# Performance work log

Hardware: AMD Instinct MI355X
Metric: run time of the kernel (lower is better)

## Reference

```python
import jax, jax.numpy as jnp
import numpy as np

E = 100000   # n_entities
R = 64       # n_relations
I = 256      # in_channels
O = 256      # out_channels
N_EDGES = 1_600_000


def setup_inputs() -> dict:
    key = jax.random.key(0)
    k1, k2, k3, k4 = jax.random.split(key, 4)
    x = jax.random.normal(k1, (E, I), dtype=jnp.float32)
    # cs must be nonzero (it is reciprocated); uniform in [0.5, 1.5)
    cs = jax.random.uniform(k2, (E, R), dtype=jnp.float32) + 0.5
    W = jax.random.normal(k3, (R, I, O), dtype=jnp.float32) * 0.05
    edge_index = jax.random.randint(k4, (2, N_EDGES), 0, E, dtype=jnp.int64)
    return {"x": x, "cs": cs, "W": W, "edge_index": edge_index}


def reference(x, cs, W, edge_index):
    # Faithful to: torch.einsum('er,rio,ej->eo', 1/cs, W, x)
    # i and j are independently contracted indices, so this factorizes:
    # out[e,o] = (sum_j x[e,j]) * sum_r (1/cs[e,r]) * (sum_i W[r,i,o])
    cs_reciprocal = 1.0 / cs                 # (E, R)
    W_sum = jnp.sum(W, axis=1)               # (R, O)
    x_sum = jnp.sum(x, axis=1)               # (E,)
    src = (cs_reciprocal @ W_sum) * x_sum[:, None]  # (E, O)
    return src
```

## Files before the change

### kernel.cpp

```cpp
#include <hip/hip_runtime.h>


constexpr int En = 100000;
constexpr int Rn = 64;
constexpr int In = 256;
constexpr int On = 256;

__global__ void wsum_kernel(const float* __restrict__ W, float* __restrict__ wsum) {
    const int r = blockIdx.x >> 3;
    const int chunk = blockIdx.x & 7;
    const int o = threadIdx.x;
    const float* base = W + ((size_t)r * In + (size_t)chunk * 32) * On + o;
    float s = 0.f;
#pragma unroll
    for (int i = 0; i < 32; ++i) s += base[(size_t)i * On];
    atomicAdd(&wsum[r * On + o], s);
}

__global__ __launch_bounds__(256) void rgcn_main(const float* __restrict__ x,
                                                 const float* __restrict__ cs,
                                                 const float* __restrict__ wsum,
                                                 float* __restrict__ out) {
    __shared__ float ldsW[Rn * On];
    __shared__ float recipT[Rn * 64];

    const int t = threadIdx.x;
    const int R0 = blockIdx.x * 64;

#pragma unroll
    for (int k = 0; k < 16; ++k) {
        const int f = k * 1024 + t * 4;
        *reinterpret_cast<float4*>(&ldsW[f]) =
            *reinterpret_cast<const float4*>(&wsum[f]);
    }

    const int wv = t >> 6;
    const int lane = t & 63;
#pragma unroll
    for (int s = 0; s < 16; ++s) {
        const int lr = s * 4 + wv;
        const int g = R0 + lr;
        float4 v = make_float4(0.f, 0.f, 0.f, 0.f);
        if (g < En)
            v = *reinterpret_cast<const float4*>(&x[(size_t)g * In + lane * 4]);
        float sum = v.x + v.y + v.z + v.w;
#pragma unroll
        for (int off = 32; off; off >>= 1) sum += __shfl_down(sum, off, 64);
        if (lane == 0) recipT[lr] = sum;
    }
    __syncthreads();

    const int q = t >> 4;
    const int m = t & 15;
    float xs[4];
    float4 c4[4];
#pragma unroll
    for (int s = 0; s < 4; ++s) {
        const int row = s * 16 + q;
        const int g = R0 + row;
        xs[s] = (g < En) ? recipT[row] : 0.f;
        c4[s] = make_float4(1.f, 1.f, 1.f, 1.f);
        if (g < En)
            c4[s] = *reinterpret_cast<const float4*>(&cs[(size_t)g * Rn + m * 4]);
    }
    __syncthreads();

#pragma unroll
    for (int s = 0; s < 4; ++s) {
        const int row = s * 16 + q;
        recipT[(4 * m + 0) * 64 + row] = xs[s] / c4[s].x;
        recipT[(4 * m + 1) * 64 + row] = xs[s] / c4[s].y;
        recipT[(4 * m + 2) * 64 + row] = xs[s] / c4[s].z;
        recipT[(4 * m + 3) * 64 + row] = xs[s] / c4[s].w;
    }
    __syncthreads();

    const int trow = t >> 5;
    const int tcol = t & 31;
    float acc[8][8];
#pragma unroll
    for (int j = 0; j < 8; ++j)
#pragma unroll
        for (int k = 0; k < 8; ++k) acc[j][k] = 0.f;

#pragma unroll 4
    for (int r = 0; r < 64; ++r) {
        const float4 a0 = *reinterpret_cast<float4*>(&recipT[r * 64 + trow * 8]);
        const float4 a1 = *reinterpret_cast<float4*>(&recipT[r * 64 + trow * 8 + 4]);
        const float4 b0 = *reinterpret_cast<float4*>(&ldsW[r * 256 + tcol * 4]);
        const float4 b1 = *reinterpret_cast<float4*>(&ldsW[r * 256 + 128 + tcol * 4]);
        const float a[8] = {a0.x, a0.y, a0.z, a0.w, a1.x, a1.y, a1.z, a1.w};
        const float b[8] = {b0.x, b0.y, b0.z, b0.w, b1.x, b1.y, b1.z, b1.w};
#pragma unroll
        for (int j = 0; j < 8; ++j)
#pragma unroll
            for (int k = 0; k < 8; ++k)
                acc[j][k] = fmaf(a[j], b[k], acc[j][k]);
    }

#pragma unroll
    for (int j = 0; j < 8; ++j) {
        const int g = R0 + trow * 8 + j;
        if (g < En) {
            const float4 o0 = make_float4(acc[j][0], acc[j][1], acc[j][2], acc[j][3]);
            const float4 o1 = make_float4(acc[j][4], acc[j][5], acc[j][6], acc[j][7]);
            *reinterpret_cast<float4*>(&out[(size_t)g * On + tcol * 4]) = o0;
            *reinterpret_cast<float4*>(&out[(size_t)g * On + 128 + tcol * 4]) = o1;
        }
    }
}

extern "C" void kernel_launch(void* const* d_in, const int* in_sizes, int n_in,
                              void* d_out, int out_size, void* d_ws, size_t ws_size,
                              hipStream_t stream) {
    const float* x  = (const float*)d_in[0];
    const float* cs = (const float*)d_in[1];
    const float* W  = (const float*)d_in[2];
    float* wsum = (float*)d_ws;
    float* out  = (float*)d_out;

    hipMemsetAsync(wsum, 0, Rn * On * sizeof(float), stream);
    wsum_kernel<<<dim3(Rn * 8), dim3(256), 0, stream>>>(W, wsum);
    const int tiles = (En + 63) / 64;
    rgcn_main<<<dim3(tiles), dim3(256), 0, stream>>>(x, cs, wsum, out);
}
```

Before: 267.7 us.

## Use bf16 MFMA for reciprocal-by-Wsum GEMM and drop atomics in W reduction

```diff
diff --git a/kernel.cpp b/kernel.cpp
--- a/kernel.cpp
+++ b/kernel.cpp
@@ -6,106 +6,156 @@
 constexpr int In = 256;
 constexpr int On = 256;
 
-__global__ void wsum_kernel(const float* __restrict__ W, float* __restrict__ wsum) {
-    const int r = blockIdx.x >> 3;
-    const int chunk = blockIdx.x & 7;
-    const int o = threadIdx.x;
-    const float* base = W + ((size_t)r * In + (size_t)chunk * 32) * On + o;
-    float s = 0.f;
-#pragma unroll
-    for (int i = 0; i < 32; ++i) s += base[(size_t)i * On];
-    atomicAdd(&wsum[r * On + o], s);
+typedef short bf16x8 __attribute__((ext_vector_type(8)));
+typedef float floatx4 __attribute__((ext_vector_type(4)));
+
+static __device__ __forceinline__ short f2bf(float f) {
+    unsigned u = __builtin_bit_cast(unsigned, f);
+    unsigned r = (u + 0x7FFFu + ((u >> 16) & 1u)) >> 16;
+    return (short)r;
 }
 
-__global__ __launch_bounds__(256) void rgcn_main(const float* __restrict__ x,
-                                                 const float* __restrict__ cs,
-                                                 const float* __restrict__ wsum,
-                                                 float* __restrict__ out) {
-    __shared__ float ldsW[Rn * On];
-    __shared__ float recipT[Rn * 64];
+__global__ __launch_bounds__(256) void wsum_partial(const float* __restrict__ W,
+                                                    float* __restrict__ partial) {
+    const int b = blockIdx.x;
+    const int r = b >> 2;
+    const int qc = b & 3;
+    const int o = threadIdx.x;
+    const float* base = W + ((size_t)r * In + (size_t)qc * 64) * On + o;
+    float s0 = 0.f, s1 = 0.f, s2 = 0.f, s3 = 0.f;
+#pragma unroll
+    for (int i = 0; i < 64; i += 4) {
+        s0 += base[(size_t)(i + 0) * On];
+        s1 += base[(size_t)(i + 1) * On];
+        s2 += base[(size_t)(i + 2) * On];
+        s3 += base[(size_t)(i + 3) * On];
+    }
+    partial[b * On + o] = (s0 + s1) + (s2 + s3);
+}
+
+__global__ __launch_bounds__(256) void wsum_combine(const float* __restrict__ partial,
+                                                    short* __restrict__ wsumT) {
+    const int r = blockIdx.x;
+    const int o = threadIdx.x;
+    const float* p = partial + (size_t)r * 4 * On + o;
+    float s = (p[0] + p[On]) + (p[2 * On] + p[3 * On]);
+    wsumT[o * Rn + r] = f2bf(s);
+}
+
+__global__ __launch_bounds__(256) void wsum_direct(const float* __restrict__ W,
+                                                   short* __restrict__ wsumT) {
+    const int r = blockIdx.x;
+    const int o = threadIdx.x;
+    const float* base = W + (size_t)r * In * On + o;
+    float s0 = 0.f, s1 = 0.f, s2 = 0.f, s3 = 0.f;
+#pragma unroll 16
+    for (int i = 0; i < 256; i += 4) {
+        s0 += base[(size_t)(i + 0) * On];
+        s1 += base[(size_t)(i + 1) * On];
+        s2 += base[(size_t)(i + 2) * On];
+        s3 += base[(size_t)(i + 3) * On];
+    }
+    wsumT[o * Rn + r] = f2bf((s0 + s1) + (s2 + s3));
+}
+
+__global__ __launch_bounds__(256, 3) void rgcn_main(const float* __restrict__ x,
+                                                    const float* __restrict__ cs,
+                                                    const short* __restrict__ wsumT,
+                                                    float* __restrict__ out) {
+    __shared__ __align__(16) short BT[On][72];
+    __shared__ __align__(16) short A[64][72];
+    __shared__ float xs[64];
 
     const int t = threadIdx.x;
     const int R0 = blockIdx.x * 64;
 
+    {
+        const floatx4* wq = (const floatx4*)wsumT;
 #pragma unroll
-    for (int k = 0; k < 16; ++k) {
-        const int f = k * 1024 + t * 4;
-        *reinterpret_cast<float4*>(&ldsW[f]) =
-            *reinterpret_cast<const float4*>(&wsum[f]);
+        for (int k = 0; k < 8; ++k) {
+            const int ch = t + 256 * k;
+            const int o = ch >> 3, seg = ch & 7;
+            *(floatx4*)((char*)&BT[o][0] + seg * 16) = wq[ch];
+        }
     }
 
-    const int wv = t >> 6;
-    const int lane = t & 63;
+    {
+        const int m = t >> 2;
+        const int kc = (t & 3) << 4;
+        const int g = R0 + m;
+        float c[16];
 #pragma unroll
-    for (int s = 0; s < 16; ++s) {
-        const int lr = s * 4 + wv;
-        const int g = R0 + lr;
-        float4 v = make_float4(0.f, 0.f, 0.f, 0.f);
-        if (g < En)
-            v = *reinterpret_cast<const float4*>(&x[(size_t)g * In + lane * 4]);
-        float sum = v.x + v.y + v.z + v.w;
+        for (int j = 0; j < 16; ++j) c[j] = 1.f;
+        if (g < En) {
+            const float4* p = (const float4*)&cs[(size_t)g * Rn + kc];
+            float4 c0 = p[0], c1 = p[1], c2 = p[2], c3 = p[3];
+            c[0] = c0.x; c[1] = c0.y; c[2] = c0.z; c[3] = c0.w;
+            c[4] = c1.x; c[5] = c1.y; c[6] = c1.z; c[7] = c1.w;
+            c[8] = c2.x; c[9] = c2.y; c[10] = c2.z; c[11] = c2.w;
+            c[12] = c3.x; c[13] = c3.y; c[14] = c3.z; c[15] = c3.w;
+        }
+        bf16x8 pk0, pk1;
 #pragma unroll
-        for (int off = 32; off; off >>= 1) sum += __shfl_down(sum, off, 64);
-        if (lane == 0) recipT[lr] = sum;
+        for (int j = 0; j < 8; ++j) {
+            pk0[j] = (g < En) ? f2bf(1.f / c[j]) : (short)0;
+            pk1[j] = (g < En) ? f2bf(1.f / c[8 + j]) : (short)0;
+        }
+        *(bf16x8*)&A[m][kc] = pk0;
+        *(bf16x8*)&A[m][kc + 8] = pk1;
     }
+
+    {
+        const int wv = t >> 6;
+        const int lane = t & 63;
+#pragma unroll
+        for (int s = 0; s < 16; ++s) {
+            const int lr = s * 4 + wv;
+            const int g = R0 + lr;
+            float4 v = make_float4(0.f, 0.f, 0.f, 0.f);
+            if (g < En)
+                v = *(const float4*)&x[(size_t)g * In + lane * 4];
+            float sum = (v.x + v.y) + (v.z + v.w);
+#pragma unroll
+            for (int off = 32; off; off >>= 1) sum += __shfl_down(sum, off, 64);
+            if (lane == 0) xs[lr] = sum;
+        }
+    }
+
     __syncthreads();
 
-    const int q = t >> 4;
-    const int m = t & 15;
-    float xs[4];
-    float4 c4[4];
+    const int wave = t >> 6;
+    const int ln = t & 63;
+    const int m0 = wave * 16;
+    const int lm = ln & 15;
+    const int q = ln >> 4;
+
+    const bf16x8 a0 = *(const bf16x8*)&A[m0 + lm][q * 8];
+    const bf16x8 a1 = *(const bf16x8*)&A[m0 + lm][32 + q * 8];
+
+    floatx4 acc[16];
 #pragma unroll
-    for (int s = 0; s < 4; ++s) {
-        const int row = s * 16 + q;
-        const int g = R0 + row;
-        xs[s] = (g < En) ? recipT[row] : 0.f;
-        c4[s] = make_float4(1.f, 1.f, 1.f, 1.f);
-        if (g < En)
-            c4[s] = *reinterpret_cast<const float4*>(&cs[(size_t)g * Rn + m * 4]);
+    for (int tile = 0; tile < 16; ++tile) {
+        const int o = tile * 16 + lm;
+        const bf16x8 b0 = *(const bf16x8*)&BT[o][q * 8];
+        const bf16x8 b1 = *(const bf16x8*)&BT[o][32 + q * 8];
+        floatx4 c = {0.f, 0.f, 0.f, 0.f};
+        c = __builtin_amdgcn_mfma_f32_16x16x32_bf16(a0, b0, c, 0, 0, 0);
+        c = __builtin_amdgcn_mfma_f32_16x16x32_bf16(a1, b1, c, 0, 0, 0);
+        acc[tile] = c;
     }
-    __syncthreads();
+
+    float xr[4];
+#pragma unroll
+    for (int rg = 0; rg < 4; ++rg) xr[rg] = xs[m0 + q * 4 + rg];
 
 #pragma unroll
-    for (int s = 0; s < 4; ++s) {
-        const int row = s * 16 + q;
-        recipT[(4 * m + 0) * 64 + row] = xs[s] / c4[s].x;
-        recipT[(4 * m + 1) * 64 + row] = xs[s] / c4[s].y;
-        recipT[(4 * m + 2) * 64 + row] = xs[s] / c4[s].z;
-        recipT[(4 * m + 3) * 64 + row] = xs[s] / c4[s].w;
-    }
-    __syncthreads();
-
-    const int trow = t >> 5;
-    const int tcol = t & 31;
-    float acc[8][8];
+    for (int tile = 0; tile < 16; ++tile) {
+        const int col = tile * 16 + lm;
 #pragma unroll
-    for (int j = 0; j < 8; ++j)
-#pragma unroll
-        for (int k = 0; k < 8; ++k) acc[j][k] = 0.f;
-
-#pragma unroll 4
-    for (int r = 0; r < 64; ++r) {
-        const float4 a0 = *reinterpret_cast<float4*>(&recipT[r * 64 + trow * 8]);
-        const float4 a1 = *reinterpret_cast<float4*>(&recipT[r * 64 + trow * 8 + 4]);
-        const float4 b0 = *reinterpret_cast<float4*>(&ldsW[r * 256 + tcol * 4]);
-        const float4 b1 = *reinterpret_cast<float4*>(&ldsW[r * 256 + 128 + tcol * 4]);
-        const float a[8] = {a0.x, a0.y, a0.z, a0.w, a1.x, a1.y, a1.z, a1.w};
-        const float b[8] = {b0.x, b0.y, b0.z, b0.w, b1.x, b1.y, b1.z, b1.w};
-#pragma unroll
-        for (int j = 0; j < 8; ++j)
-#pragma unroll
-            for (int k = 0; k < 8; ++k)
-                acc[j][k] = fmaf(a[j], b[k], acc[j][k]);
-    }
-
-#pragma unroll
-    for (int j = 0; j < 8; ++j) {
-        const int g = R0 + trow * 8 + j;
-        if (g < En) {
-            const float4 o0 = make_float4(acc[j][0], acc[j][1], acc[j][2], acc[j][3]);
-            const float4 o1 = make_float4(acc[j][4], acc[j][5], acc[j][6], acc[j][7]);
-            *reinterpret_cast<float4*>(&out[(size_t)g * On + tcol * 4]) = o0;
-            *reinterpret_cast<float4*>(&out[(size_t)g * On + 128 + tcol * 4]) = o1;
+        for (int rg = 0; rg < 4; ++rg) {
+            const int row = R0 + m0 + q * 4 + rg;
+            if (row < En)
+                out[(size_t)row * On + col] = acc[tile][rg] * xr[rg];
         }
     }
 }
@@ -116,11 +166,18 @@
     const float* x  = (const float*)d_in[0];
     const float* cs = (const float*)d_in[1];
     const float* W  = (const float*)d_in[2];
-    float* wsum = (float*)d_ws;
-    float* out  = (float*)d_out;
+    float* out = (float*)d_out;
 
-    hipMemsetAsync(wsum, 0, Rn * On * sizeof(float), stream);
-    wsum_kernel<<<dim3(Rn * 8), dim3(256), 0, stream>>>(W, wsum);
+    short* wsumT = (short*)d_ws;
+    float* partial = (float*)((char*)d_ws + 32768);
+
+    if (ws_size >= (size_t)(32768 + 256 * On * 4)) {
+        wsum_partial<<<dim3(256), dim3(256), 0, stream>>>(W, partial);
+        wsum_combine<<<dim3(64), dim3(256), 0, stream>>>(partial, wsumT);
+    } else {
+        wsum_direct<<<dim3(64), dim3(256), 0, stream>>>(W, wsumT);
+    }
+
     const int tiles = (En + 63) / 64;
-    rgcn_main<<<dim3(tiles), dim3(256), 0, stream>>>(x, cs, wsum, out);
+    rgcn_main<<<dim3(tiles), dim3(256), 0, stream>>>(x, cs, wsumT, out);
 }
```

Measured after the change: 239.5 us. 1.12x faster.
